# Performance work log

Measured on AMD Instinct MI355X. Metric: run time of the kernel, lower is better.

## Reference

```python
import jax, jax.numpy as jnp
import numpy as np

D = 128  # input_dim

def setup_inputs() -> dict:
    key = jax.random.key(0)
    ks = jax.random.split(key, 9)
    B, Lq, Lkv = 4, 4096, 4096
    s = 1.0 / np.sqrt(D)
    return {
        "x1": jax.random.normal(ks[0], (B, Lq, D), dtype=jnp.float32),
        "x2": jax.random.normal(ks[1], (B, Lkv, D), dtype=jnp.float32),
        "x3": jax.random.normal(ks[2], (B, Lkv, D), dtype=jnp.float32),
        "Wq": jax.random.normal(ks[3], (D, D), dtype=jnp.float32) * s,
        "bq": jax.random.normal(ks[4], (D,), dtype=jnp.float32) * s,
        "Wk": jax.random.normal(ks[5], (D, D), dtype=jnp.float32) * s,
        "bk": jax.random.normal(ks[6], (D,), dtype=jnp.float32) * s,
        "Wv": jax.random.normal(ks[7], (D, D), dtype=jnp.float32) * s,
        "bv": jax.random.normal(ks[8], (D,), dtype=jnp.float32) * s,
    }

def reference(x1, x2, x3, Wq, bq, Wk, bk, Wv, bv):
    # torch Linear: y = x @ W.T + b
    q = jnp.einsum('bld,ed->ble', x1, Wq) + bq  # [B,Lq,D]
    k = jnp.einsum('bld,ed->ble', x2, Wk) + bk  # [B,Lkv,D]
    v = jnp.einsum('bld,ed->ble', x3, Wv) + bv  # [B,Lkv,D]
    scores = jnp.einsum('bqd,bkd->bqk', q, k) / jnp.sqrt(jnp.float32(x1.shape[-1]))
    attn = jax.nn.softmax(scores, axis=2)
    return jnp.einsum('bqk,bkd->bqd', attn, v)
```

## Files before the change

### kernel.cpp

```cpp
#include <hip/hip_runtime.h>
#include <hip/hip_bf16.h>

typedef __attribute__((ext_vector_type(8))) short short8;
typedef __attribute__((ext_vector_type(4))) float v4f;
typedef __attribute__((ext_vector_type(16))) float v16f;

__device__ __forceinline__ unsigned short f2bf(float f) {
    union { float f; unsigned u; } c; c.f = f;
    unsigned r = c.u + 0x7FFFu + ((c.u >> 16) & 1u);
    return (unsigned short)(r >> 16);
}
__device__ __forceinline__ unsigned cvtpk(float a, float b) {
    unsigned r;
    asm("v_cvt_pk_bf16_f32 %0, %1, %2" : "=v"(r) : "v"(a), "v"(b));
    return r;
}
__device__ __forceinline__ void plswap(unsigned& a, unsigned& b) {
    asm("v_permlane32_swap_b32 %0, %1" : "+v"(a), "+v"(b));
}
__device__ __forceinline__ float bf2f(unsigned short h) {
    union { unsigned u; float f; } c; c.u = ((unsigned)h) << 16;
    return c.f;
}
__device__ __forceinline__ v16f zero16() {
    v16f z;
#pragma unroll
    for (int i = 0; i < 16; i++) z[i] = 0.f;
    return z;
}

__device__ __forceinline__ void g2l16(const unsigned short* g, unsigned short* l) {
    __builtin_amdgcn_global_load_lds(
        (const __attribute__((address_space(1))) unsigned int*)g,
        (__attribute__((address_space(3))) unsigned int*)l,
        16, 0, 0);
}

__global__ __launch_bounds__(512) void proj_kernel(
    const float* __restrict__ x1, const float* __restrict__ x2, const float* __restrict__ x3,
    const float* __restrict__ Wq, const float* __restrict__ bq,
    const float* __restrict__ Wk, const float* __restrict__ bk,
    const float* __restrict__ Wv, const float* __restrict__ bv,
    unsigned short* __restrict__ qb, unsigned short* __restrict__ kb,
    unsigned short* __restrict__ vb, float qscale)
{
    __shared__ __attribute__((aligned(16))) unsigned short Xs[16384];
    __shared__ __attribute__((aligned(16))) unsigned short Ws[16384];

    int tid = threadIdx.x;
    int wave = tid >> 6, lane = tid & 63;
    int lmod = lane & 15, ldiv = lane >> 4;
    int p = blockIdx.x % 3;
    int row0 = (blockIdx.x / 3) * 128;

    const float* X = p == 0 ? x1 : p == 1 ? x2 : x3;
    const float* W = p == 0 ? Wq : p == 1 ? Wk : Wv;
    const float* bias = p == 0 ? bq : p == 1 ? bk : bv;
    float scale = p == 0 ? qscale : 1.0f;

#pragma unroll
    for (int i = 0; i < 8; i++) {
        int c = tid + i * 512;
        int row = c >> 5, d0 = (c & 31) * 4;
        v4f f = *(const v4f*)(X + (size_t)(row0 + row) * 128 + d0);
        int off = ((row >> 4) * 16 + (d0 >> 5) * 4 + ((d0 >> 3) & 3)) * 128 + (row & 15) * 8 + (d0 & 7);
        *(uint2*)&Xs[off] = make_uint2(cvtpk(f[0], f[1]), cvtpk(f[2], f[3]));
        v4f g = *(const v4f*)(W + (size_t)row * 128 + d0);
        *(uint2*)&Ws[off] = make_uint2(cvtpk(g[0], g[1]), cvtpk(g[2], g[3]));
    }
    __syncthreads();

    short8 af[4];
#pragma unroll
    for (int kc = 0; kc < 4; kc++)
        af[kc] = *(const short8*)&Xs[wave * 2048 + (kc * 4 + ldiv) * 128 + lmod * 8];

#pragma unroll
    for (int ct = 0; ct < 8; ct++) {
        v4f acc = {0.f, 0.f, 0.f, 0.f};
#pragma unroll
        for (int kc = 0; kc < 4; kc++) {
            short8 bf = *(const short8*)&Ws[ct * 2048 + (kc * 4 + ldiv) * 128 + lmod * 8];
            acc = __builtin_amdgcn_mfma_f32_16x16x32_bf16(af[kc], bf, acc, 0, 0, 0);
        }
        int e = ct * 16 + lmod;
        float bv_ = bias[e];
#pragma unroll
        for (int r = 0; r < 4; r++) {
            int orow = row0 + wave * 16 + ldiv * 4 + r;
            unsigned short h = f2bf((acc[r] + bv_) * scale);
            if (p == 0) {
                qb[(size_t)orow * 128 + e] = h;
            } else if (p == 1) {
                int b = orow >> 12, key = orow & 4095, kk = key & 31;
                kb[b * 524288 + (key >> 5) * 4096
                   + (e >> 4) * 512 + (kk + ((e >> 3) & 1) * 32) * 8 + (e & 7)] = h;
            } else {
                int b = orow >> 12, key = orow & 4095, kk = key & 31;
                vb[b * 524288 + (key >> 5) * 4096
                   + (e >> 5) * 1024 + ((kk >> 4) & 1) * 512
                   + ((e & 31) + ((kk >> 3) & 1) * 32) * 8 + (kk & 7)] = h;
            }
        }
    }
}

__global__ __launch_bounds__(256, 3) void attn_kernel(
    const unsigned short* __restrict__ Qb,
    const unsigned short* __restrict__ Kb,
    const unsigned short* __restrict__ Vb,
    unsigned short* __restrict__ Opart,
    float* __restrict__ Lbuf)
{
    __shared__ __attribute__((aligned(16))) unsigned short Kt[2][4096];
    __shared__ __attribute__((aligned(16))) unsigned short Vt[2][4096];

    int tid = threadIdx.x;
    int wave = tid >> 6, lane = tid & 63;
    int lq = lane & 31, lhi = lane >> 5;
    int split = blockIdx.x % 12;
    int qidx = blockIdx.x / 12;
    int b = qidx >> 5;
    int q0 = (qidx & 31) * 128 + wave * 32;

    int t0 = (split * 32) / 3;
    int t1 = ((split + 1) * 32) / 3;

    short8 qf[8];
    {
        const unsigned short* qptr = Qb + (size_t)(b * 4096 + q0 + lq) * 128 + lhi * 8;
#pragma unroll
        for (int s = 0; s < 8; s++) qf[s] = *(const short8*)(qptr + s * 16);
    }

    v16f oacc[4];
#pragma unroll
    for (int dt = 0; dt < 4; dt++) oacc[dt] = zero16();
    float lsum = 0.f;

    const unsigned short* kbb = Kb + b * 524288;
    const unsigned short* vbb = Vb + b * 524288;

#pragma unroll
    for (int i = 0; i < 2; i++) {
        g2l16(kbb + t0 * 4096 + wave * 1024 + i * 512 + lane * 8, &Kt[0][wave * 1024 + i * 512]);
        g2l16(vbb + t0 * 4096 + wave * 1024 + i * 512 + lane * 8, &Vt[0][wave * 1024 + i * 512]);
    }
    __syncthreads();

    for (int t = t0; t < t1; t++) {
        int cur = (t - t0) & 1;
        if (t + 1 < t1) {
            const unsigned short* kg = kbb + (t + 1) * 4096;
            const unsigned short* vg = vbb + (t + 1) * 4096;
#pragma unroll
            for (int i = 0; i < 2; i++) {
                g2l16(kg + wave * 1024 + i * 512 + lane * 8, &Kt[cur ^ 1][wave * 1024 + i * 512]);
                g2l16(vg + wave * 1024 + i * 512 + lane * 8, &Vt[cur ^ 1][wave * 1024 + i * 512]);
            }
        }

        v16f s0 = zero16(), s1 = zero16();
        __builtin_amdgcn_s_setprio(1);
#pragma unroll
        for (int s = 0; s < 4; s++) {
            short8 kf0 = *(const short8*)&Kt[cur][(2 * s) * 512 + lane * 8];
            short8 kf1 = *(const short8*)&Kt[cur][(2 * s + 1) * 512 + lane * 8];
            s0 = __builtin_amdgcn_mfma_f32_32x32x16_bf16(kf0, qf[2 * s], s0, 0, 0, 0);
            s1 = __builtin_amdgcn_mfma_f32_32x32x16_bf16(kf1, qf[2 * s + 1], s1, 0, 0, 0);
        }
        __builtin_amdgcn_s_setprio(0);

        unsigned c[8];
        float ls = 0.f;
#pragma unroll
        for (int i = 0; i < 8; i++) {
            float ea = __builtin_amdgcn_exp2f(s0[2 * i] + s1[2 * i]);
            float eb = __builtin_amdgcn_exp2f(s0[2 * i + 1] + s1[2 * i + 1]);
            ls += ea + eb;
            c[i] = cvtpk(ea, eb);
        }
        lsum += ls;
        plswap(c[0], c[2]); plswap(c[1], c[3]);
        plswap(c[4], c[6]); plswap(c[5], c[7]);
        short8 pf0, pf1;
        {
            unsigned* u0 = (unsigned*)&pf0;
            u0[0] = c[0]; u0[1] = c[1]; u0[2] = c[2]; u0[3] = c[3];
            unsigned* u1 = (unsigned*)&pf1;
            u1[0] = c[4]; u1[1] = c[5]; u1[2] = c[6]; u1[3] = c[7];
        }

        __builtin_amdgcn_s_setprio(1);
#pragma unroll
        for (int dt = 0; dt < 4; dt++) {
            short8 vf0 = *(const short8*)&Vt[cur][dt * 1024 + lane * 8];
            short8 vf1 = *(const short8*)&Vt[cur][dt * 1024 + 512 + lane * 8];
            oacc[dt] = __builtin_amdgcn_mfma_f32_32x32x16_bf16(pf0, vf0, oacc[dt], 0, 0, 0);
            oacc[dt] = __builtin_amdgcn_mfma_f32_32x32x16_bf16(pf1, vf1, oacc[dt], 0, 0, 0);
        }
        __builtin_amdgcn_s_setprio(0);
        __syncthreads();
    }

    lsum += __shfl_xor(lsum, 32);
    int gqb = b * 4096 + q0;
    if (lane < 32) Lbuf[split * 16384 + gqb + lq] = lsum;

#pragma unroll
    for (int r = 0; r < 16; r++) {
        int q = (r & 3) + (r >> 2) * 8 + 4 * lhi;
        unsigned short* obase = Opart + (size_t)(split * 16384 + gqb + q) * 128 + lq;
#pragma unroll
        for (int dt = 0; dt < 4; dt++)
            obase[dt * 32] = f2bf(oacc[dt][r]);
    }
}

__global__ __launch_bounds__(256) void merge_kernel(
    const unsigned short* __restrict__ Opart,
    const float* __restrict__ Lbuf,
    float* __restrict__ Out)
{
    int t = blockIdx.x * 256 + threadIdx.x;
#pragma unroll
    for (int it = 0; it < 2; it++) {
        int base = (t + it * 131072) * 8;
        int q = base >> 7;
        float lacc = 0.f;
#pragma unroll
        for (int s = 0; s < 12; s++) lacc += Lbuf[s * 16384 + q];
        float inv = 1.0f / lacc;
        float acc[8] = {0.f, 0.f, 0.f, 0.f, 0.f, 0.f, 0.f, 0.f};
#pragma unroll
        for (int s = 0; s < 12; s++) {
            short8 o = *(const short8*)(Opart + (size_t)s * 2097152 + base);
#pragma unroll
            for (int j = 0; j < 8; j++) acc[j] += bf2f((unsigned short)o[j]);
        }
        v4f lo = {acc[0] * inv, acc[1] * inv, acc[2] * inv, acc[3] * inv};
        v4f hi = {acc[4] * inv, acc[5] * inv, acc[6] * inv, acc[7] * inv};
        *(v4f*)(Out + base) = lo;
        *(v4f*)(Out + base + 4) = hi;
    }
}

extern "C" void kernel_launch(void* const* d_in, const int* in_sizes, int n_in,
                              void* d_out, int out_size, void* d_ws, size_t ws_size,
                              hipStream_t stream) {
    const float* x1 = (const float*)d_in[0];
    const float* x2 = (const float*)d_in[1];
    const float* x3 = (const float*)d_in[2];
    const float* Wq = (const float*)d_in[3];
    const float* bq = (const float*)d_in[4];
    const float* Wk = (const float*)d_in[5];
    const float* bk = (const float*)d_in[6];
    const float* Wv = (const float*)d_in[7];
    const float* bv = (const float*)d_in[8];
    float* out = (float*)d_out;

    unsigned short* qb = (unsigned short*)d_ws;
    unsigned short* kb = qb + (size_t)2097152;
    unsigned short* vb = kb + (size_t)2097152;
    unsigned short* op = vb + (size_t)2097152;
    float* lb = (float*)(op + (size_t)25165824);

    const float qscale = 1.4426950408889634f / 11.313708498984761f;

    proj_kernel<<<384, 512, 0, stream>>>(x1, x2, x3, Wq, bq, Wk, bk, Wv, bv,
                                         qb, kb, vb, qscale);
    attn_kernel<<<1536, 256, 0, stream>>>(qb, kb, vb, op, lb);
    merge_kernel<<<512, 256, 0, stream>>>(op, lb, out);
}
```

Before: 144.5 us.

## Use single-wave attention blocks reading K/V fragments directly from global memory

The attention kernel drops the LDS double-buffered K/V staging and block-wide barriers. Each block is now one wave that loads its MFMA fragments straight from global memory, relying on L2 for reuse across waves. The two interleaved score accumulators are merged into one serial MFMA chain. This removes the LDS traffic and the __syncthreads stalls, but gives up explicit prefetch overlap and sharing within a block, adds a dependent MFMA chain, and puts four times the K/V load requests on the cache hierarchy.

```diff
diff --git a/kernel.cpp b/kernel.cpp
--- a/kernel.cpp
+++ b/kernel.cpp
@@ -27,13 +27,6 @@
 #pragma unroll
     for (int i = 0; i < 16; i++) z[i] = 0.f;
     return z;
-}
-
-__device__ __forceinline__ void g2l16(const unsigned short* g, unsigned short* l) {
-    __builtin_amdgcn_global_load_lds(
-        (const __attribute__((address_space(1))) unsigned int*)g,
-        (__attribute__((address_space(3))) unsigned int*)l,
-        16, 0, 0);
 }
 
 __global__ __launch_bounds__(512) void proj_kernel(
@@ -105,23 +98,19 @@
     }
 }
 
-__global__ __launch_bounds__(256, 3) void attn_kernel(
+__global__ __launch_bounds__(64, 3) void attn_kernel(
     const unsigned short* __restrict__ Qb,
     const unsigned short* __restrict__ Kb,
     const unsigned short* __restrict__ Vb,
     unsigned short* __restrict__ Opart,
     float* __restrict__ Lbuf)
 {
-    __shared__ __attribute__((aligned(16))) unsigned short Kt[2][4096];
-    __shared__ __attribute__((aligned(16))) unsigned short Vt[2][4096];
-
-    int tid = threadIdx.x;
-    int wave = tid >> 6, lane = tid & 63;
+    int lane = threadIdx.x;
     int lq = lane & 31, lhi = lane >> 5;
     int split = blockIdx.x % 12;
-    int qidx = blockIdx.x / 12;
-    int b = qidx >> 5;
-    int q0 = (qidx & 31) * 128 + wave * 32;
+    int qw = blockIdx.x / 12;
+    int b = qw >> 7;
+    int q0 = (qw & 127) * 32;
 
     int t0 = (split * 32) / 3;
     int t1 = ((split + 1) * 32) / 3;
@@ -138,36 +127,19 @@
     for (int dt = 0; dt < 4; dt++) oacc[dt] = zero16();
     float lsum = 0.f;
 
-    const unsigned short* kbb = Kb + b * 524288;
-    const unsigned short* vbb = Vb + b * 524288;
-
-#pragma unroll
-    for (int i = 0; i < 2; i++) {
-        g2l16(kbb + t0 * 4096 + wave * 1024 + i * 512 + lane * 8, &Kt[0][wave * 1024 + i * 512]);
-        g2l16(vbb + t0 * 4096 + wave * 1024 + i * 512 + lane * 8, &Vt[0][wave * 1024 + i * 512]);
-    }
-    __syncthreads();
+    const unsigned short* kbb = Kb + b * 524288 + lane * 8;
+    const unsigned short* vbb = Vb + b * 524288 + lane * 8;
 
     for (int t = t0; t < t1; t++) {
-        int cur = (t - t0) & 1;
-        if (t + 1 < t1) {
-            const unsigned short* kg = kbb + (t + 1) * 4096;
-            const unsigned short* vg = vbb + (t + 1) * 4096;
-#pragma unroll
-            for (int i = 0; i < 2; i++) {
-                g2l16(kg + wave * 1024 + i * 512 + lane * 8, &Kt[cur ^ 1][wave * 1024 + i * 512]);
-                g2l16(vg + wave * 1024 + i * 512 + lane * 8, &Vt[cur ^ 1][wave * 1024 + i * 512]);
-            }
-        }
-
-        v16f s0 = zero16(), s1 = zero16();
+        const unsigned short* kt = kbb + t * 4096;
+        const unsigned short* vt = vbb + t * 4096;
+
+        v16f s = zero16();
         __builtin_amdgcn_s_setprio(1);
 #pragma unroll
-        for (int s = 0; s < 4; s++) {
-            short8 kf0 = *(const short8*)&Kt[cur][(2 * s) * 512 + lane * 8];
-            short8 kf1 = *(const short8*)&Kt[cur][(2 * s + 1) * 512 + lane * 8];
-            s0 = __builtin_amdgcn_mfma_f32_32x32x16_bf16(kf0, qf[2 * s], s0, 0, 0, 0);
-            s1 = __builtin_amdgcn_mfma_f32_32x32x16_bf16(kf1, qf[2 * s + 1], s1, 0, 0, 0);
+        for (int sc = 0; sc < 8; sc++) {
+            short8 kf = *(const short8*)(kt + sc * 512);
+            s = __builtin_amdgcn_mfma_f32_32x32x16_bf16(kf, qf[sc], s, 0, 0, 0);
         }
         __builtin_amdgcn_s_setprio(0);
 
@@ -175,8 +147,8 @@
         float ls = 0.f;
 #pragma unroll
         for (int i = 0; i < 8; i++) {
-            float ea = __builtin_amdgcn_exp2f(s0[2 * i] + s1[2 * i]);
-            float eb = __builtin_amdgcn_exp2f(s0[2 * i + 1] + s1[2 * i + 1]);
+            float ea = __builtin_amdgcn_exp2f(s[2 * i]);
+            float eb = __builtin_amdgcn_exp2f(s[2 * i + 1]);
             ls += ea + eb;
             c[i] = cvtpk(ea, eb);
         }
@@ -194,13 +166,12 @@
         __builtin_amdgcn_s_setprio(1);
 #pragma unroll
         for (int dt = 0; dt < 4; dt++) {
-            short8 vf0 = *(const short8*)&Vt[cur][dt * 1024 + lane * 8];
-            short8 vf1 = *(const short8*)&Vt[cur][dt * 1024 + 512 + lane * 8];
+            short8 vf0 = *(const short8*)(vt + dt * 1024);
+            short8 vf1 = *(const short8*)(vt + dt * 1024 + 512);
             oacc[dt] = __builtin_amdgcn_mfma_f32_32x32x16_bf16(pf0, vf0, oacc[dt], 0, 0, 0);
             oacc[dt] = __builtin_amdgcn_mfma_f32_32x32x16_bf16(pf1, vf1, oacc[dt], 0, 0, 0);
         }
         __builtin_amdgcn_s_setprio(0);
-        __syncthreads();
     }
 
     lsum += __shfl_xor(lsum, 32);
@@ -269,6 +240,6 @@
 
     proj_kernel<<<384, 512, 0, stream>>>(x1, x2, x3, Wq, bq, Wk, bk, Wv, bv,
                                          qb, kb, vb, qscale);
-    attn_kernel<<<1536, 256, 0, stream>>>(qb, kb, vb, op, lb);
+    attn_kernel<<<6144, 64, 0, stream>>>(qb, kb, vb, op, lb);
     merge_kernel<<<512, 256, 0, stream>>>(op, lb, out);
 }
```

Measured after the change: 158.5 us. +9.7%, slower.
